# Optimization experiments

Hardware: AMD Instinct MI355X
Metric: run time of the kernel (lower is better)

## Reference

```python
import jax, jax.numpy as jnp
import numpy as np

N = 100000
E = 1600000
IN_DIM = 128
HID = 64
NCOMM = 32


def setup_inputs() -> dict:
    key = jax.random.key(0)
    k = jax.random.split(key, 8)
    x = jax.random.normal(k[0], (N, IN_DIM), dtype=jnp.float32)
    edge_index = jax.random.randint(k[1], (2, E), 0, N, dtype=jnp.int64)
    s1 = 1.0 / np.sqrt(IN_DIM)
    s2 = 1.0 / np.sqrt(HID)
    W1 = jax.random.uniform(k[2], (IN_DIM, HID), jnp.float32, -s1, s1)
    b1 = jnp.zeros((HID,), jnp.float32)
    W2 = jax.random.uniform(k[3], (HID, HID), jnp.float32, -s2, s2)
    b2 = jnp.zeros((HID,), jnp.float32)
    Wfc = jax.random.uniform(k[4], (HID, NCOMM), jnp.float32, -s2, s2)
    bfc = jax.random.uniform(k[5], (NCOMM,), jnp.float32, -s2, s2)
    return {"x": x, "edge_index": edge_index, "W1": W1, "b1": b1,
            "W2": W2, "b2": b2, "Wfc": Wfc, "bfc": bfc}


def gcn_conv(x, row, col, norm, W, b):
    # PyG GCNConv: linear -> gather(source) * norm -> scatter_add(target) -> + bias
    h = x @ W                                    # [N, out]
    msgs = h[row] * norm[:, None]                # [E+N, out] gather (memory-bound)
    agg = jax.ops.segment_sum(msgs, col, num_segments=x.shape[0])
    return agg + b


def reference(x, edge_index, W1, b1, W2, b2, Wfc, bfc):
    n = x.shape[0]
    # add self-loops (PyG GCNConv default)
    loop = jnp.arange(n, dtype=edge_index.dtype)
    row = jnp.concatenate([edge_index[0], loop])  # source
    col = jnp.concatenate([edge_index[1], loop])  # target
    # symmetric normalization D^{-1/2} (A+I) D^{-1/2}
    deg = jax.ops.segment_sum(jnp.ones_like(col, dtype=x.dtype), col, num_segments=n)
    dinv = jnp.where(deg > 0, jax.lax.rsqrt(deg), 0.0)
    norm = dinv[row] * dinv[col]
    h = jax.nn.relu(gcn_conv(x, row, col, norm, W1, b1))   # dropout = identity (eval)
    h = jax.nn.relu(gcn_conv(h, row, col, norm, W2, b2))
    return jax.nn.sigmoid(h @ Wfc + bfc)
```

## Files before the change

kernel.cpp:

```cpp
#include <hip/hip_runtime.h>
#include <hip/hip_fp16.h>
#include <math.h>

#define N_NODES 100000
#define N_EDGES 1600000
#define IN_DIM  128
#define HID     64
#define NCOMM   32
#define NB        391
#define BSHIFT    8
#define BCAP      6144
#define EPB       2048
#define NBIN_BLK  782

typedef _Float16 f16x8 __attribute__((ext_vector_type(8)));
typedef float    f32x4 __attribute__((ext_vector_type(4)));

__device__ __forceinline__ int load_idx(const int* e32, long long pos, int is64) {
  if (is64) return (int)(((const long long*)e32)[pos]);
  return e32[pos];
}

__global__ __launch_bounds__(512) void k_init(int* __restrict__ bcnt, int* __restrict__ zrow) {
  int t = threadIdx.x;
  if (t < NB) bcnt[t] = 0;
  if (t >= 480) zrow[t - 480] = 0;
}

__global__ __launch_bounds__(256) void k_bin(const int* __restrict__ e, int* __restrict__ bcnt,
                                             unsigned* __restrict__ ebuf) {
  __shared__ int cnt[NB];
  __shared__ int base[NB];
  __shared__ int s_hi;
  if (threadIdx.x == 0) s_hi = 0;
  for (int i = threadIdx.x; i < NB; i += 256) cnt[i] = 0;
  __syncthreads();
  if (((const unsigned*)e)[2 * threadIdx.x + 1] != 0u) atomicOr(&s_hi, 1);
  __syncthreads();
  const int is64 = (s_hi == 0);
  long long eb = (long long)blockIdx.x * EPB;
  int rr[EPB / 256], cc[EPB / 256], lr[EPB / 256];
  #pragma unroll
  for (int j = 0; j < EPB / 256; ++j) {
    long long eid = eb + j * 256 + threadIdx.x;
    if (eid < N_EDGES) {
      rr[j] = load_idx(e, eid, is64);
      cc[j] = load_idx(e, (long long)N_EDGES + eid, is64);
      lr[j] = atomicAdd(&cnt[cc[j] >> BSHIFT], 1);
    }
  }
  __syncthreads();
  for (int b = threadIdx.x; b < NB; b += 256)
    base[b] = cnt[b] ? atomicAdd(&bcnt[b], cnt[b]) : 0;
  __syncthreads();
  #pragma unroll
  for (int j = 0; j < EPB / 256; ++j) {
    long long eid = eb + j * 256 + threadIdx.x;
    if (eid < N_EDGES) {
      int bb = cc[j] >> BSHIFT;
      int pos = bb * BCAP + base[bb] + lr[j];
      ebuf[pos] = ((unsigned)(cc[j] & 255) << 17) | (unsigned)rr[j];
    }
  }
}

__global__ __launch_bounds__(512) void k_degsort(const unsigned* __restrict__ ebuf, const int* __restrict__ bcnt,
                                                 float* __restrict__ dinv, int2* __restrict__ parr,
                                                 int* __restrict__ srow) {
  __shared__ int cnt[256];
  __shared__ int scn[256];
  __shared__ int cur[256];
  __shared__ unsigned eds[BCAP];
  int t = threadIdx.x;
  int b = blockIdx.x;
  int c0 = b << BSHIFT;
  int n = bcnt[b];
  if (t < 256) cnt[t] = 0;
  __syncthreads();
  for (int i = t; i < n; i += 512) {
    unsigned w = ebuf[b * BCAP + i];
    eds[i] = w;
    atomicAdd(&cnt[w >> 17], 1);
  }
  __syncthreads();
  int d = (t < 256) ? cnt[t] : 0;
  if (t < 256) scn[t] = d;
  __syncthreads();
  for (int off = 1; off < 256; off <<= 1) {
    int u = (t >= off && t < 256) ? scn[t - off] : 0;
    __syncthreads();
    if (t < 256) scn[t] += u;
    __syncthreads();
  }
  if (t < 256) {
    int sabs = b * BCAP + scn[t] - d;
    int node = c0 + t;
    if (node < N_NODES) {
      dinv[node] = rsqrtf((float)d + 1.0f);
      parr[node] = make_int2(sabs, sabs + d);
    }
    cur[t] = sabs;
  }
  __syncthreads();
  for (int i = t; i < n; i += 512) {
    unsigned w = eds[i];
    int pos = atomicAdd(&cur[w >> 17], 1);
    srow[pos] = (int)(w & 0x1FFFFu);
  }
}

template<int K, int M, bool FINAL, bool INH>
__global__ __launch_bounds__(256) void k_mfma(const void* __restrict__ X, const float* __restrict__ W,
                                              void* __restrict__ Y, const float* __restrict__ bias,
                                              const float* __restrict__ dscale) {
  constexpr int NN = M / 16;
  constexpr int KS = K / 32;
  __shared__ char smem[M * K * 2];

  const int tid = threadIdx.x;
  for (int i = tid; i < K * M / 4; i += 256) {
    int k  = i / (M / 4);
    int mf = (i % (M / 4)) * 4;
    float4 wv = *(const float4*)(W + (size_t)k * M + mf);
    float wa[4] = {wv.x, wv.y, wv.z, wv.w};
    #pragma unroll
    for (int c = 0; c < 4; ++c) {
      int m = mf + c;
      int byte_off = m * (2 * K) + ((((k >> 3) << 4)) ^ ((m & 7) << 4)) + (k & 7) * 2;
      *(_Float16*)(smem + byte_off) = (_Float16)wa[c];
    }
  }
  __syncthreads();

  const int lane = tid & 63;
  const int wv_  = tid >> 6;
  const int rowbase = blockIdx.x * 128 + wv_ * 32;
  const int lr = lane & 15;
  const int kg = lane >> 4;
  const int r0 = rowbase + lr;
  const int r1 = r0 + 16;
  const int rc0 = (r0 < N_NODES) ? r0 : (N_NODES - 1);
  const int rc1 = (r1 < N_NODES) ? r1 : (N_NODES - 1);

  f32x4 acc[2][NN] = {};

  #pragma unroll
  for (int ks = 0; ks < KS; ++ks) {
    const int k0 = ks * 32 + kg * 8;
    f16x8 a0, a1;
    if constexpr (!INH) {
      const float* xr = (const float*)X;
      float4 u0 = *(const float4*)(xr + (size_t)rc0 * K + k0);
      float4 u1 = *(const float4*)(xr + (size_t)rc0 * K + k0 + 4);
      float4 u2 = *(const float4*)(xr + (size_t)rc1 * K + k0);
      float4 u3 = *(const float4*)(xr + (size_t)rc1 * K + k0 + 4);
      a0[0] = (_Float16)u0.x; a0[1] = (_Float16)u0.y; a0[2] = (_Float16)u0.z; a0[3] = (_Float16)u0.w;
      a0[4] = (_Float16)u1.x; a0[5] = (_Float16)u1.y; a0[6] = (_Float16)u1.z; a0[7] = (_Float16)u1.w;
      a1[0] = (_Float16)u2.x; a1[1] = (_Float16)u2.y; a1[2] = (_Float16)u2.z; a1[3] = (_Float16)u2.w;
      a1[4] = (_Float16)u3.x; a1[5] = (_Float16)u3.y; a1[6] = (_Float16)u3.z; a1[7] = (_Float16)u3.w;
    } else {
      const char* xb = (const char*)X;
      a0 = *(const f16x8*)(xb + (size_t)rc0 * (2 * K) + k0 * 2);
      a1 = *(const f16x8*)(xb + (size_t)rc1 * (2 * K) + k0 * 2);
    }
    const int slot = (k0 >> 3) << 4;
    #pragma unroll
    for (int n = 0; n < NN; ++n) {
      const int col = n * 16 + lr;
      f16x8 b = *(const f16x8*)(smem + col * (2 * K) + (slot ^ ((col & 7) << 4)));
      acc[0][n] = __builtin_amdgcn_mfma_f32_16x16x32_f16(a0, b, acc[0][n], 0, 0, 0);
      acc[1][n] = __builtin_amdgcn_mfma_f32_16x16x32_f16(a1, b, acc[1][n], 0, 0, 0);
    }
  }

  #pragma unroll
  for (int m2 = 0; m2 < 2; ++m2) {
    #pragma unroll
    for (int r = 0; r < 4; ++r) {
      const int row = rowbase + m2 * 16 + kg * 4 + r;
      if (row < N_NODES) {
        float ds = FINAL ? 0.f : dscale[row];
        #pragma unroll
        for (int n = 0; n < NN; ++n) {
          const int col = n * 16 + lr;
          float v = acc[m2][n][r];
          if constexpr (FINAL) {
            v += bias[col];
            v = 1.f / (1.f + __expf(-v));
            ((float*)Y)[(size_t)row * M + col] = v;
          } else {
            ((__half*)Y)[(size_t)row * M + col] = __float2half(v * ds);
          }
        }
      }
    }
  }
}

__device__ __forceinline__ void addrow(float* acc, uint4 h) {
  __half2 p0 = *(__half2*)&h.x;
  __half2 p1 = *(__half2*)&h.y;
  __half2 p2 = *(__half2*)&h.z;
  __half2 p3 = *(__half2*)&h.w;
  float2 f0 = __half22float2(p0);
  float2 f1 = __half22float2(p1);
  float2 f2 = __half22float2(p2);
  float2 f3 = __half22float2(p3);
  acc[0] += f0.x; acc[1] += f0.y;
  acc[2] += f1.x; acc[3] += f1.y;
  acc[4] += f2.x; acc[5] += f2.y;
  acc[6] += f3.x; acc[7] += f3.y;
}

__global__ __launch_bounds__(256) void k_agg(const __half* __restrict__ H, __half* __restrict__ O,
                                             const int2* __restrict__ parr, const int* __restrict__ srow,
                                             const float* __restrict__ dinv, const float* __restrict__ bias) {
  int wid  = (blockIdx.x * 256 + threadIdx.x) >> 6;
  int lane = threadIdx.x & 63;
  if (wid >= N_NODES) return;
  const int q  = lane >> 3;
  const int fl = lane & 7;
  const char* Hb = (const char*)H;
  int2 se = parr[wid];
  int s = se.x, e = se.y;
  float acc[8] = {0.f, 0.f, 0.f, 0.f, 0.f, 0.f, 0.f, 0.f};
  for (int j = s; j < e; j += 16) {
    int i0 = j + q;
    int i1 = j + 8 + q;
    int r0 = srow[i0];
    int r1 = srow[i1];
    r0 = (i0 < e) ? r0 : N_NODES;
    r1 = (i1 < e) ? r1 : N_NODES;
    uint4 h0 = *(const uint4*)(Hb + (size_t)((unsigned)r0 * 128u + (unsigned)fl * 16u));
    uint4 h1 = *(const uint4*)(Hb + (size_t)((unsigned)r1 * 128u + (unsigned)fl * 16u));
    addrow(acc, h0);
    addrow(acc, h1);
  }
  if (q == 0) {
    uint4 hb = *(const uint4*)(Hb + (size_t)((unsigned)wid * 128u + (unsigned)fl * 16u));
    addrow(acc, hb);
  }
  #pragma unroll
  for (int m = 8; m < 64; m <<= 1) {
    #pragma unroll
    for (int i = 0; i < 8; ++i) acc[i] += __shfl_xor(acc[i], m, 64);
  }
  if (lane < 8) {
    float di = dinv[wid];
    float4 ba = ((const float4*)bias)[2 * fl + 0];
    float4 bb = ((const float4*)bias)[2 * fl + 1];
    __half2 o0 = __floats2half2_rn(fmaxf(acc[0] * di + ba.x, 0.f), fmaxf(acc[1] * di + ba.y, 0.f));
    __half2 o1 = __floats2half2_rn(fmaxf(acc[2] * di + ba.z, 0.f), fmaxf(acc[3] * di + ba.w, 0.f));
    __half2 o2 = __floats2half2_rn(fmaxf(acc[4] * di + bb.x, 0.f), fmaxf(acc[5] * di + bb.y, 0.f));
    __half2 o3 = __floats2half2_rn(fmaxf(acc[6] * di + bb.z, 0.f), fmaxf(acc[7] * di + bb.w, 0.f));
    uint4 pv;
    pv.x = *(unsigned*)&o0;
    pv.y = *(unsigned*)&o1;
    pv.z = *(unsigned*)&o2;
    pv.w = *(unsigned*)&o3;
    *(uint4*)((char*)O + (size_t)wid * (HID * 2) + fl * 16) = pv;
  }
}

extern "C" void kernel_launch(void* const* d_in, const int* in_sizes, int n_in,
                              void* d_out, int out_size, void* d_ws, size_t ws_size,
                              hipStream_t stream) {
  const float* x   = (const float*)d_in[0];
  const int*   e   = (const int*)d_in[1];
  const float* W1  = (const float*)d_in[2];
  const float* b1  = (const float*)d_in[3];
  const float* W2  = (const float*)d_in[4];
  const float* b2  = (const float*)d_in[5];
  const float* Wfc = (const float*)d_in[6];
  const float* bfc = (const float*)d_in[7];
  float* out = (float*)d_out;

  char* ws = (char*)d_ws;
  __half*   hbuf = (__half*)  (ws);
  unsigned* ebuf = (unsigned*)(ws);
  int*      srow = (int*)     (ws + 12800192);
  __half*   abuf = (__half*)  (ws + 22409472);
  float*    dinv = (float*)   (ws + 35209472);
  int2*     parr = (int2*)    (ws + 35609472);
  int*      bcnt = (int*)     (ws + 36409536);

  k_init<<<1, 512, 0, stream>>>(bcnt, (int*)(ws + (size_t)N_NODES * 128));
  k_bin<<<NBIN_BLK, 256, 0, stream>>>(e, bcnt, ebuf);
  k_degsort<<<NB, 512, 0, stream>>>(ebuf, bcnt, dinv, parr, srow);

  const int gBlocks = (N_NODES + 127) / 128;
  k_mfma<IN_DIM, HID, false, false><<<gBlocks, 256, 0, stream>>>(x, W1, hbuf, nullptr, dinv);
  k_agg<<<N_NODES * 64 / 256, 256, 0, stream>>>(hbuf, abuf, parr, srow, dinv, b1);
  k_mfma<HID, HID, false, true><<<gBlocks, 256, 0, stream>>>(abuf, W2, hbuf, nullptr, dinv);
  k_agg<<<N_NODES * 64 / 256, 256, 0, stream>>>(hbuf, abuf, parr, srow, dinv, b2);
  k_mfma<HID, NCOMM, true, true><<<gBlocks, 256, 0, stream>>>(abuf, Wfc, out, bfc, nullptr);
}
```

Before: 187.1 us.

## Fuse next-layer dense matmuls into aggregation kernels with multi-node waves

The separate MFMA kernels for the second GCN linear layer and the final classifier are removed. Their dense products are now done inside the aggregation kernel: after each node's neighbour sum, bias and ReLU, the wave multiplies the row by register-held weights and reduces across lanes with shuffles. Each wave handles 16 nodes so the weight loads are amortised. This saves two kernel launches and the round trip of intermediate activations through memory, at the cost of scalar FMA work and extra shuffles in a gather-bound kernel and fewer waves in flight.

```diff
diff --git a/kernel.cpp b/kernel.cpp
--- a/kernel.cpp
+++ b/kernel.cpp
@@ -12,6 +12,7 @@
 #define BCAP      6144
 #define EPB       2048
 #define NBIN_BLK  782
+#define NPW       16
 
 typedef _Float16 f16x8 __attribute__((ext_vector_type(8)));
 typedef float    f32x4 __attribute__((ext_vector_type(4)));
@@ -21,10 +22,11 @@
   return e32[pos];
 }
 
-__global__ __launch_bounds__(512) void k_init(int* __restrict__ bcnt, int* __restrict__ zrow) {
+__global__ __launch_bounds__(512) void k_init(int* __restrict__ bcnt, int* __restrict__ z1,
+                                              int* __restrict__ z2) {
   int t = threadIdx.x;
   if (t < NB) bcnt[t] = 0;
-  if (t >= 480) zrow[t - 480] = 0;
+  if (t < 32) { z1[t] = 0; z2[t] = 0; }
 }
 
 __global__ __launch_bounds__(256) void k_bin(const int* __restrict__ e, int* __restrict__ bcnt,
@@ -109,10 +111,9 @@
   }
 }
 
-template<int K, int M, bool FINAL, bool INH>
-__global__ __launch_bounds__(256) void k_mfma(const void* __restrict__ X, const float* __restrict__ W,
-                                              void* __restrict__ Y, const float* __restrict__ bias,
-                                              const float* __restrict__ dscale) {
+template<int K, int M>
+__global__ __launch_bounds__(256) void k_mfma(const float* __restrict__ X, const float* __restrict__ W,
+                                              __half* __restrict__ Y, const float* __restrict__ dscale) {
   constexpr int NN = M / 16;
   constexpr int KS = K / 32;
   __shared__ char smem[M * K * 2];
@@ -148,21 +149,14 @@
   for (int ks = 0; ks < KS; ++ks) {
     const int k0 = ks * 32 + kg * 8;
     f16x8 a0, a1;
-    if constexpr (!INH) {
-      const float* xr = (const float*)X;
-      float4 u0 = *(const float4*)(xr + (size_t)rc0 * K + k0);
-      float4 u1 = *(const float4*)(xr + (size_t)rc0 * K + k0 + 4);
-      float4 u2 = *(const float4*)(xr + (size_t)rc1 * K + k0);
-      float4 u3 = *(const float4*)(xr + (size_t)rc1 * K + k0 + 4);
-      a0[0] = (_Float16)u0.x; a0[1] = (_Float16)u0.y; a0[2] = (_Float16)u0.z; a0[3] = (_Float16)u0.w;
-      a0[4] = (_Float16)u1.x; a0[5] = (_Float16)u1.y; a0[6] = (_Float16)u1.z; a0[7] = (_Float16)u1.w;
-      a1[0] = (_Float16)u2.x; a1[1] = (_Float16)u2.y; a1[2] = (_Float16)u2.z; a1[3] = (_Float16)u2.w;
-      a1[4] = (_Float16)u3.x; a1[5] = (_Float16)u3.y; a1[6] = (_Float16)u3.z; a1[7] = (_Float16)u3.w;
-    } else {
-      const char* xb = (const char*)X;
-      a0 = *(const f16x8*)(xb + (size_t)rc0 * (2 * K) + k0 * 2);
-      a1 = *(const f16x8*)(xb + (size_t)rc1 * (2 * K) + k0 * 2);
-    }
+    float4 u0 = *(const float4*)(X + (size_t)rc0 * K + k0);
+    float4 u1 = *(const float4*)(X + (size_t)rc0 * K + k0 + 4);
+    float4 u2 = *(const float4*)(X + (size_t)rc1 * K + k0);
+    float4 u3 = *(const float4*)(X + (size_t)rc1 * K + k0 + 4);
+    a0[0] = (_Float16)u0.x; a0[1] = (_Float16)u0.y; a0[2] = (_Float16)u0.z; a0[3] = (_Float16)u0.w;
+    a0[4] = (_Float16)u1.x; a0[5] = (_Float16)u1.y; a0[6] = (_Float16)u1.z; a0[7] = (_Float16)u1.w;
+    a1[0] = (_Float16)u2.x; a1[1] = (_Float16)u2.y; a1[2] = (_Float16)u2.z; a1[3] = (_Float16)u2.w;
+    a1[4] = (_Float16)u3.x; a1[5] = (_Float16)u3.y; a1[6] = (_Float16)u3.z; a1[7] = (_Float16)u3.w;
     const int slot = (k0 >> 3) << 4;
     #pragma unroll
     for (int n = 0; n < NN; ++n) {
@@ -179,18 +173,11 @@
     for (int r = 0; r < 4; ++r) {
       const int row = rowbase + m2 * 16 + kg * 4 + r;
       if (row < N_NODES) {
-        float ds = FINAL ? 0.f : dscale[row];
+        float ds = dscale[row];
         #pragma unroll
         for (int n = 0; n < NN; ++n) {
           const int col = n * 16 + lr;
-          float v = acc[m2][n][r];
-          if constexpr (FINAL) {
-            v += bias[col];
-            v = 1.f / (1.f + __expf(-v));
-            ((float*)Y)[(size_t)row * M + col] = v;
-          } else {
-            ((__half*)Y)[(size_t)row * M + col] = __float2half(v * ds);
-          }
+          Y[(size_t)row * M + col] = __float2half(acc[m2][n][r] * ds);
         }
       }
     }
@@ -212,53 +199,107 @@
   acc[6] += f3.x; acc[7] += f3.y;
 }
 
-__global__ __launch_bounds__(256) void k_agg(const __half* __restrict__ H, __half* __restrict__ O,
-                                             const int2* __restrict__ parr, const int* __restrict__ srow,
-                                             const float* __restrict__ dinv, const float* __restrict__ bias) {
-  int wid  = (blockIdx.x * 256 + threadIdx.x) >> 6;
-  int lane = threadIdx.x & 63;
-  if (wid >= N_NODES) return;
+template<int MOUT, bool FINAL>
+__global__ __launch_bounds__(256) void k_aggf(const __half* __restrict__ H, void* __restrict__ O,
+                                              const int2* __restrict__ parr, const int* __restrict__ srow,
+                                              const float* __restrict__ dinv, const float* __restrict__ bpre,
+                                              const float* __restrict__ Wn, const float* __restrict__ bfin) {
+  constexpr int J = MOUT / 8;
+  int gw = (blockIdx.x * 256 + threadIdx.x) >> 6;
+  int nb = gw * NPW;
+  if (nb >= N_NODES) return;
+  const int lane = threadIdx.x & 63;
   const int q  = lane >> 3;
   const int fl = lane & 7;
   const char* Hb = (const char*)H;
-  int2 se = parr[wid];
-  int s = se.x, e = se.y;
-  float acc[8] = {0.f, 0.f, 0.f, 0.f, 0.f, 0.f, 0.f, 0.f};
-  for (int j = s; j < e; j += 16) {
-    int i0 = j + q;
-    int i1 = j + 8 + q;
-    int r0 = srow[i0];
-    int r1 = srow[i1];
-    r0 = (i0 < e) ? r0 : N_NODES;
-    r1 = (i1 < e) ? r1 : N_NODES;
-    uint4 h0 = *(const uint4*)(Hb + (size_t)((unsigned)r0 * 128u + (unsigned)fl * 16u));
-    uint4 h1 = *(const uint4*)(Hb + (size_t)((unsigned)r1 * 128u + (unsigned)fl * 16u));
-    addrow(acc, h0);
-    addrow(acc, h1);
-  }
-  if (q == 0) {
-    uint4 hb = *(const uint4*)(Hb + (size_t)((unsigned)wid * 128u + (unsigned)fl * 16u));
-    addrow(acc, hb);
-  }
-  #pragma unroll
-  for (int m = 8; m < 64; m <<= 1) {
-    #pragma unroll
-    for (int i = 0; i < 8; ++i) acc[i] += __shfl_xor(acc[i], m, 64);
-  }
-  if (lane < 8) {
-    float di = dinv[wid];
-    float4 ba = ((const float4*)bias)[2 * fl + 0];
-    float4 bb = ((const float4*)bias)[2 * fl + 1];
-    __half2 o0 = __floats2half2_rn(fmaxf(acc[0] * di + ba.x, 0.f), fmaxf(acc[1] * di + ba.y, 0.f));
-    __half2 o1 = __floats2half2_rn(fmaxf(acc[2] * di + ba.z, 0.f), fmaxf(acc[3] * di + ba.w, 0.f));
-    __half2 o2 = __floats2half2_rn(fmaxf(acc[4] * di + bb.x, 0.f), fmaxf(acc[5] * di + bb.y, 0.f));
-    __half2 o3 = __floats2half2_rn(fmaxf(acc[6] * di + bb.z, 0.f), fmaxf(acc[7] * di + bb.w, 0.f));
-    uint4 pv;
-    pv.x = *(unsigned*)&o0;
-    pv.y = *(unsigned*)&o1;
-    pv.z = *(unsigned*)&o2;
-    pv.w = *(unsigned*)&o3;
-    *(uint4*)((char*)O + (size_t)wid * (HID * 2) + fl * 16) = pv;
+
+  float wgt[8][J];
+  #pragma unroll
+  for (int i = 0; i < 8; ++i) {
+    if constexpr (MOUT == 64) {
+      float4 wa = *(const float4*)(Wn + (8 * fl + i) * 64 + 8 * q);
+      float4 wb = *(const float4*)(Wn + (8 * fl + i) * 64 + 8 * q + 4);
+      wgt[i][0] = wa.x; wgt[i][1] = wa.y; wgt[i][2] = wa.z; wgt[i][3] = wa.w;
+      wgt[i][4] = wb.x; wgt[i][5] = wb.y; wgt[i][6] = wb.z; wgt[i][7] = wb.w;
+    } else {
+      float4 wa = *(const float4*)(Wn + (8 * fl + i) * 32 + 4 * q);
+      wgt[i][0] = wa.x; wgt[i][1] = wa.y; wgt[i][2] = wa.z; wgt[i][3] = wa.w;
+    }
+  }
+  float bp[8];
+  {
+    float4 ba = *(const float4*)(bpre + 8 * fl);
+    float4 bb = *(const float4*)(bpre + 8 * fl + 4);
+    bp[0] = ba.x; bp[1] = ba.y; bp[2] = ba.z; bp[3] = ba.w;
+    bp[4] = bb.x; bp[5] = bb.y; bp[6] = bb.z; bp[7] = bb.w;
+  }
+  float4 bf = {0.f, 0.f, 0.f, 0.f};
+  if constexpr (FINAL) bf = *(const float4*)(bfin + 4 * q);
+
+  for (int jn = 0; jn < NPW; ++jn) {
+    const int node = nb + jn;
+    int2 se = parr[node];
+    int s = se.x, e = se.y;
+    float acc[8] = {0.f, 0.f, 0.f, 0.f, 0.f, 0.f, 0.f, 0.f};
+    for (int j = s; j < e; j += 16) {
+      int i0 = j + q;
+      int i1 = j + 8 + q;
+      int r0 = srow[i0];
+      int r1 = srow[i1];
+      r0 = (i0 < e) ? r0 : N_NODES;
+      r1 = (i1 < e) ? r1 : N_NODES;
+      uint4 h0 = *(const uint4*)(Hb + (size_t)((unsigned)r0 * 128u + (unsigned)fl * 16u));
+      uint4 h1 = *(const uint4*)(Hb + (size_t)((unsigned)r1 * 128u + (unsigned)fl * 16u));
+      addrow(acc, h0);
+      addrow(acc, h1);
+    }
+    if (q == 0) {
+      uint4 hb = *(const uint4*)(Hb + (size_t)((unsigned)node * 128u + (unsigned)fl * 16u));
+      addrow(acc, hb);
+    }
+    #pragma unroll
+    for (int m = 8; m < 64; m <<= 1) {
+      #pragma unroll
+      for (int i = 0; i < 8; ++i) acc[i] += __shfl_xor(acc[i], m, 64);
+    }
+    const float di = dinv[node];
+    float row[8];
+    #pragma unroll
+    for (int i = 0; i < 8; ++i) row[i] = fmaxf(acc[i] * di + bp[i], 0.f);
+    float p[J];
+    #pragma unroll
+    for (int jj = 0; jj < J; ++jj) p[jj] = 0.f;
+    #pragma unroll
+    for (int i = 0; i < 8; ++i) {
+      #pragma unroll
+      for (int jj = 0; jj < J; ++jj) p[jj] += row[i] * wgt[i][jj];
+    }
+    #pragma unroll
+    for (int m = 1; m < 8; m <<= 1) {
+      #pragma unroll
+      for (int jj = 0; jj < J; ++jj) p[jj] += __shfl_xor(p[jj], m, 64);
+    }
+    if (fl == 0) {
+      if constexpr (FINAL) {
+        float4 o;
+        o.x = 1.f / (1.f + __expf(-(p[0] + bf.x)));
+        o.y = 1.f / (1.f + __expf(-(p[1] + bf.y)));
+        o.z = 1.f / (1.f + __expf(-(p[2] + bf.z)));
+        o.w = 1.f / (1.f + __expf(-(p[3] + bf.w)));
+        *(float4*)((float*)O + (size_t)node * NCOMM + 4 * q) = o;
+      } else {
+        __half2 o0 = __floats2half2_rn(p[0] * di, p[1] * di);
+        __half2 o1 = __floats2half2_rn(p[2] * di, p[3] * di);
+        __half2 o2 = __floats2half2_rn(p[4] * di, p[5] * di);
+        __half2 o3 = __floats2half2_rn(p[6] * di, p[7] * di);
+        uint4 pv;
+        pv.x = *(unsigned*)&o0;
+        pv.y = *(unsigned*)&o1;
+        pv.z = *(unsigned*)&o2;
+        pv.w = *(unsigned*)&o3;
+        *(uint4*)((char*)O + (size_t)node * 128 + q * 16) = pv;
+      }
+    }
   }
 }
 
@@ -276,22 +317,20 @@
   float* out = (float*)d_out;
 
   char* ws = (char*)d_ws;
-  __half*   hbuf = (__half*)  (ws);
-  unsigned* ebuf = (unsigned*)(ws);
-  int*      srow = (int*)     (ws + 12800192);
-  __half*   abuf = (__half*)  (ws + 22409472);
-  float*    dinv = (float*)   (ws + 35209472);
-  int2*     parr = (int2*)    (ws + 35609472);
-  int*      bcnt = (int*)     (ws + 36409536);
-
-  k_init<<<1, 512, 0, stream>>>(bcnt, (int*)(ws + (size_t)N_NODES * 128));
+  __half*   hbuf1 = (__half*)  (ws);
+  unsigned* ebuf  = (unsigned*)(ws);
+  int*      srow  = (int*)     (ws + 12800192);
+  __half*   hbuf2 = (__half*)  (ws + 22409472);
+  float*    dinv  = (float*)   (ws + 35209600);
+  int2*     parr  = (int2*)    (ws + 35609600);
+  int*      bcnt  = (int*)     (ws + 36409600);
+
+  k_init<<<1, 512, 0, stream>>>(bcnt, (int*)(ws + (size_t)N_NODES * 128),
+                                (int*)(ws + 22409472 + (size_t)N_NODES * 128));
   k_bin<<<NBIN_BLK, 256, 0, stream>>>(e, bcnt, ebuf);
   k_degsort<<<NB, 512, 0, stream>>>(ebuf, bcnt, dinv, parr, srow);
 
-  const int gBlocks = (N_NODES + 127) / 128;
-  k_mfma<IN_DIM, HID, false, false><<<gBlocks, 256, 0, stream>>>(x, W1, hbuf, nullptr, dinv);
-  k_agg<<<N_NODES * 64 / 256, 256, 0, stream>>>(hbuf, abuf, parr, srow, dinv, b1);
-  k_mfma<HID, HID, false, true><<<gBlocks, 256, 0, stream>>>(abuf, W2, hbuf, nullptr, dinv);
-  k_agg<<<N_NODES * 64 / 256, 256, 0, stream>>>(hbuf, abuf, parr, srow, dinv, b2);
-  k_mfma<HID, NCOMM, true, true><<<gBlocks, 256, 0, stream>>>(abuf, Wfc, out, bfc, nullptr);
-}
+  k_mfma<IN_DIM, HID><<<(N_NODES + 127) / 128, 256, 0, stream>>>(x, W1, hbuf1, dinv);
+  k_aggf<HID, false><<<(N_NODES / NPW + 3) / 4, 256, 0, stream>>>(hbuf1, hbuf2, parr, srow, dinv, b1, W2, nullptr);
+  k_aggf<NCOMM, true><<<(N_NODES / NPW + 3) / 4, 256, 0, stream>>>(hbuf2, out, parr, srow, dinv, b2, Wfc, bfc);
+}
```

After: 246.1 us. +31.5%, slower.
